# Kernel tuning notes

Hardware: AMD Instinct MI355X
Metric: run time of the kernel (lower is better)

The kernel has to match this reference:

```python
import jax, jax.numpy as jnp
from jax import lax
import numpy as np

MAX_ITER = 200      # hard-coded in DyanEncoder.forward
N_REWEIGHT = 3      # outer reweighting rounds
EPS_W = 0.01


def build_dictionary(rr, theta, T):
    # rows i=0..T-1: [1, rr^i*cos(i*th), (-rr)^i*cos(i*th), rr^i*sin(i*th), (-rr)^i*sin(i*th)]
    i = jnp.arange(T, dtype=rr.dtype)[:, None]          # [T,1]
    pow_p = jnp.power(rr[None, :], i)                   # rr^i, [T,N]
    sign = 1.0 - 2.0 * (jnp.arange(T) % 2).astype(rr.dtype)[:, None]
    pow_m = sign * pow_p                                # (-rr)^i
    c = jnp.cos(i * theta[None, :])
    s = jnp.sin(i * theta[None, :])
    ones = jnp.ones((T, 1), dtype=rr.dtype)
    return jnp.concatenate([ones, pow_p * c, pow_m * c, pow_p * s, pow_m * s], axis=1)  # [T, 1+4N]


def fista_reweighted(D, Y, lam, w):
    # D: [T,K], Y: [B,T,P], w: broadcastable to [B,K,P]
    DtD = D.T @ D                                       # [K,K]
    DtY = jnp.einsum('tk,btp->bkp', D, Y)               # [B,K,P]
    L = jnp.linalg.norm(DtD, ord=2)                     # spectral norm
    Linv = 1.0 / L
    # torch uses Linv.data.item() here -> detached scalar
    w_lam = w * lam * lax.stop_gradient(Linv)
    K = DtD.shape[1]
    A = jnp.eye(K, dtype=D.dtype) - DtD * Linv
    c_minus = DtY * Linv - w_lam
    c_plus = DtY * Linv + w_lam
    x0 = jnp.zeros_like(DtY)

    def step(carry, _):
        x_old, y_old, t_old = carry
        Ay = jnp.einsum('kj,bjp->bkp', A, y_old)
        x_new = jnp.maximum(0.0, Ay + c_minus) + jnp.minimum(0.0, Ay + c_plus)
        t_new = (1.0 + jnp.sqrt(1.0 + 4.0 * t_old ** 2)) / 2.0
        y_new = x_new + ((t_old - 1.0) / t_new) * (x_new - x_old)
        return (x_new, y_new, t_new), None

    (x_fin, _, _), _ = lax.scan(step, (x0, x0, jnp.float32(1.0)), None, length=MAX_ITER)
    return x_fin


def setup_inputs() -> dict:
    key = jax.random.key(0)
    k1, k2, k3 = jax.random.split(key, 3)
    Npoles = 160
    B, T, P = 1, 36, 512
    x = jax.random.normal(k1, (B, T, P), dtype=jnp.float32)
    rr = jax.random.uniform(k2, (Npoles,), dtype=jnp.float32)            # pole magnitudes in (0,1)
    theta = jax.random.uniform(k3, (Npoles,), dtype=jnp.float32) * 3.1415927  # pole angles
    return {"x": x, "rr": rr, "theta": theta, "T": T}


def reference(x, rr, theta, T):
    lam = 0.1
    dic = build_dictionary(rr, theta, T)                # [T, K]
    K = dic.shape[1]
    B, _, P = x.shape
    w = jnp.ones((1, K, P), dtype=x.dtype)
    final = None
    for _ in range(N_REWEIGHT):
        temp = fista_reweighted(dic, x, lam, w)         # [B,K,P]
        wr = 1.0 / (jnp.abs(temp) + EPS_W)
        w = wr / jnp.linalg.norm(wr.reshape(-1))
        final = temp
    return final, dic
```

## Files before the change

kernel.cpp:

```cpp
#include <hip/hip_runtime.h>
#include <math.h>

#define TT 36
#define NP 160
#define KDIM 641
#define PP 512
#define KPAD 704
#define NU 321
#define NSLOT 384
#define BT 512
#define NW 8
#define LAM 0.1f
#define EPSW 0.01f
#define NITER 200
#define NPOW 160

__global__ void k_build_dic(const float* __restrict__ rr, const float* __restrict__ th,
                            float* __restrict__ D, float* __restrict__ outD) {
  int idx = blockIdx.x * blockDim.x + threadIdx.x;
  if (idx >= TT * KDIM) return;
  int t = idx / KDIM, k = idx % KDIM;
  float v;
  if (k == 0) {
    v = 1.0f;
  } else {
    int g = (k - 1) / NP;
    int p = (k - 1) % NP;
    float ft = (float)t;
    float pw = powf(rr[p], ft);
    if ((g == 1 || g == 3) && (t & 1)) pw = -pw;
    float ang = ft * th[p];
    v = pw * ((g < 2) ? cosf(ang) : sinf(ang));
  }
  D[idx] = v;
  outD[idx] = v;
}

__global__ void k_G(const float* __restrict__ D, float* __restrict__ G) {
  int idx = blockIdx.x * blockDim.x + threadIdx.x;
  if (idx >= TT * TT) return;
  int i = idx / TT, j = idx % TT;
  float s = 0.0f;
  for (int k = 0; k < KDIM; ++k) s = fmaf(D[i * KDIM + k], D[j * KDIM + k], s);
  G[idx] = s;
}

__global__ void k_power(const float* __restrict__ G, float* __restrict__ Lb,
                        float* __restrict__ mug) {
  int lane = threadIdx.x;
  float g[TT];
#pragma unroll
  for (int j = 0; j < TT; ++j) g[j] = (lane < TT) ? G[lane * TT + j] : 0.0f;
  float v = (lane < TT) ? 1.0f : 0.0f;
  for (int it = 0; it < NPOW; ++it) {
    float u = 0.0f;
#pragma unroll
    for (int j = 0; j < TT; ++j) u = fmaf(g[j], __shfl(v, j, 64), u);
    float s = u * u;
#pragma unroll
    for (int o = 32; o >= 1; o >>= 1) s += __shfl_xor(s, o, 64);
    v = u * rsqrtf(s);
  }
  float u = 0.0f;
#pragma unroll
  for (int j = 0; j < TT; ++j) u = fmaf(g[j], __shfl(v, j, 64), u);
  float num = v * u, den = v * v;
#pragma unroll
  for (int o = 32; o >= 1; o >>= 1) {
    num += __shfl_xor(num, o, 64);
    den += __shfl_xor(den, o, 64);
  }
  if (lane == 0) {
    float L = num / den;
    Lb[0] = L;
    Lb[1] = 1.0f / L;
    Lb[3] = 0.0f;
    float t = 1.0f;
    for (int i = 0; i < NITER; ++i) {
      float tn = 0.5f * (1.0f + sqrtf(1.0f + 4.0f * t * t));
      mug[i] = (t - 1.0f) / tn;
      t = tn;
    }
  }
}

template <int C>
__device__ __forceinline__ float dppadd(float v) {
  int t = __builtin_amdgcn_update_dpp(0, __float_as_int(v), C, 0xf, 0xf, true);
  return v + __int_as_float(t);
}
__device__ __forceinline__ float wave_sum63(float v) {
  v = dppadd<0xB1>(v);
  v = dppadd<0x4E>(v);
  v = dppadd<0x141>(v);
  v = dppadd<0x140>(v);
  v = dppadd<0x142>(v);
  v = dppadd<0x143>(v);
  return v;
}

__device__ __forceinline__ int colmap(int u) {
  return (u == 0) ? 0 : ((u < 161) ? u : u + 160);
}

__global__ __launch_bounds__(BT, 1) void k_round(
    const float* __restrict__ Dg, const float* __restrict__ X,
    float* __restrict__ Lb, const float* __restrict__ mug,
    const float* __restrict__ xprev, float* __restrict__ xout,
    int first, int last) {
  __shared__ __align__(16) float2 ylds2[NSLOT];
  __shared__ float pbuf[NW * NSLOT];
  __shared__ float muLDS[NITER];
  __shared__ float rn[NW];

  const int tid  = threadIdx.x;
  const int lane = tid & 63;
  const int w    = tid >> 6;
  const float sgn = (w & 1) ? -1.0f : 1.0f;
  const int p    = blockIdx.x;

  const float Linv = Lb[1];
  const float sqL  = sqrtf(Linv);
  const float lamL = LAM * Linv;

  const bool act = (tid < NU);
  const int u    = act ? tid : 0;
  const int kP   = colmap(u);
  const int kM   = (u == 0) ? 0 : kP + 160;

  float Dq[5][6];
#pragma unroll
  for (int i = 0; i < 5; ++i)
#pragma unroll
    for (int j = 0; j < 6; ++j) {
      const int t = w + 8 * i;
      const int ua = lane + 64 * j;
      Dq[i][j] = (t < TT && ua < NU) ? Dg[t * KDIM + colmap(ua)] * sqL : 0.0f;
    }

  float cmP, cpP, cmM, cpM;
  {
    float sE0 = 0.f, sO0 = 0.f;
#pragma unroll 6
    for (int t = 0; t < TT; ++t) {
      const float dv = act ? Dg[t * KDIM + kP] : 0.0f;
      const float xv = X[t * PP + p];
      if (t & 1) sO0 = fmaf(dv, xv, sO0);
      else       sE0 = fmaf(dv, xv, sE0);
    }
    const float c0P = (sE0 + sO0) * Linv, c0M = (sE0 - sO0) * Linv;
    float wlP = lamL, wlM = lamL;
    if (!first) {
      const float nl = lamL * Lb[2];
      wlP = nl / (fabsf(xprev[p * KPAD + kP]) + EPSW);
      wlM = nl / (fabsf(xprev[p * KPAD + ((u > 0) ? kM : kP)]) + EPSW);
    }
    cmP = c0P - wlP; cpP = c0P + wlP;
    cmM = c0M - wlM; cpM = c0M + wlM;
  }

  if (tid < NSLOT) ylds2[tid] = make_float2(0.f, 0.f);
  if (tid < NITER) muLDS[tid] = mug[tid];

  float xP = 0.f, xM = 0.f, yP = 0.f, yM = 0.f;

  __syncthreads();

  for (int it = 0; it < NITER; ++it) {
    float acc[5] = {0.f, 0.f, 0.f, 0.f, 0.f};
#pragma unroll
    for (int j = 0; j < 6; ++j) {
      const float2 yv = ylds2[lane + 64 * j];
      const float op = fmaf(sgn, yv.y, yv.x);
#pragma unroll
      for (int i = 0; i < 5; ++i) acc[i] = fmaf(Dq[i][j], op, acc[i]);
    }
    float z[5];
#pragma unroll
    for (int i = 0; i < 5; ++i) {
      const float r = wave_sum63(acc[i]);
      z[i] = __int_as_float(__builtin_amdgcn_readlane(__float_as_int(r), 63));
    }
#pragma unroll
    for (int j = 0; j < 6; ++j) {
      float pw = Dq[0][j] * z[0];
#pragma unroll
      for (int i = 1; i < 5; ++i) pw = fmaf(Dq[i][j], z[i], pw);
      pbuf[w * NSLOT + lane + 64 * j] = pw;
    }
    __syncthreads();

    const float mu = muLDS[it];
    if (act) {
      const float sE = (pbuf[0 * NSLOT + u] + pbuf[2 * NSLOT + u])
                     + (pbuf[4 * NSLOT + u] + pbuf[6 * NSLOT + u]);
      const float sO = (pbuf[1 * NSLOT + u] + pbuf[3 * NSLOT + u])
                     + (pbuf[5 * NSLOT + u] + pbuf[7 * NSLOT + u]);
      const float sP = sE + sO, sM = sE - sO;
      float uu, xn;
      uu = yP - sP; xn = fmaxf(0.f, uu + cmP) + fminf(0.f, uu + cpP);
      yP = fmaf(mu, xn - xP, xn); xP = xn;
      uu = yM - sM; xn = fmaxf(0.f, uu + cmM) + fminf(0.f, uu + cpM);
      yM = fmaf(mu, xn - xM, xn); xM = xn;
      ylds2[u] = make_float2(yP, (u > 0) ? yM : 0.0f);
    }
    __syncthreads();
  }

  if (act) {
    if (last) {
      xout[kP * PP + p] = xP;
      if (u > 0) xout[kM * PP + p] = xM;
    } else {
      xout[p * KPAD + kP] = xP;
      if (u > 0) xout[p * KPAD + kM] = xM;
    }
  }

  if (!last) {
    float s = 0.0f;
    if (act) {
      const float rP = 1.0f / (fabsf(xP) + EPSW);
      s = rP * rP;
      if (u > 0) { const float rM = 1.0f / (fabsf(xM) + EPSW); s += rM * rM; }
    }
    s = wave_sum63(s);
    if (lane == 63) rn[w] = s;
    __syncthreads();
    if (tid == 0) {
      float tot = 0.f;
#pragma unroll
      for (int i = 0; i < NW; ++i) tot += rn[i];
      atomicAdd(&Lb[3], tot);
    }
  }
}

__global__ void k_norm(float* __restrict__ Lb) {
  if (threadIdx.x == 0) {
    Lb[2] = 1.0f / sqrtf(Lb[3]);
    Lb[3] = 0.0f;
  }
}

extern "C" void kernel_launch(void* const* d_in, const int* in_sizes, int n_in,
                              void* d_out, int out_size, void* d_ws, size_t ws_size,
                              hipStream_t stream) {
  const float* x  = (const float*)d_in[0];
  const float* rr = (const float*)d_in[1];
  const float* th = (const float*)d_in[2];
  float* out = (float*)d_out;
  float* ws  = (float*)d_ws;

  size_t off = 0;
  auto alloc = [&](size_t n) {
    float* p = ws + off;
    off += (n + 63) & ~(size_t)63;
    return p;
  };
  float* D    = alloc((size_t)TT * KDIM);
  float* G    = alloc(TT * TT);
  float* Lb   = alloc(16);
  float* mug  = alloc(NITER);
  float* xa   = alloc((size_t)PP * KPAD);
  if (off * sizeof(float) > ws_size) return;

  k_build_dic<<<(TT * KDIM + 255) / 256, 256, 0, stream>>>(rr, th, D, out + (size_t)KDIM * PP);
  k_G<<<(TT * TT + 255) / 256, 256, 0, stream>>>(D, G);
  k_power<<<1, 64, 0, stream>>>(G, Lb, mug);

  for (int r = 0; r < 3; ++r) {
    const int first = (r == 0), last = (r == 2);
    float* xo = last ? out : xa;
    k_round<<<PP, BT, 0, stream>>>(D, x, Lb, mug, xa, xo, first, last);
    if (!last) k_norm<<<1, 64, 0, stream>>>(Lb);
  }
}
```

Measured before the change: 748.3 us.

## Fuse three reweighting rounds into one persistent kernel with grid barrier

Measured after the change: 825.8 us. 10.3% more time.

```diff
diff --git a/kernel.cpp b/kernel.cpp
--- a/kernel.cpp
+++ b/kernel.cpp
@@ -5,7 +5,6 @@
 #define NP 160
 #define KDIM 641
 #define PP 512
-#define KPAD 704
 #define NU 321
 #define NSLOT 384
 #define BT 512
@@ -75,6 +74,9 @@
     Lb[0] = L;
     Lb[1] = 1.0f / L;
     Lb[3] = 0.0f;
+    Lb[4] = 0.0f;
+    ((unsigned*)(Lb + 8))[0] = 0u;
+    ((unsigned*)(Lb + 8))[1] = 0u;
     float t = 1.0f;
     for (int i = 0; i < NITER; ++i) {
       float tn = 0.5f * (1.0f + sqrtf(1.0f + 4.0f * t * t));
@@ -103,15 +105,15 @@
   return (u == 0) ? 0 : ((u < 161) ? u : u + 160);
 }
 
-__global__ __launch_bounds__(BT, 1) void k_round(
+__global__ __launch_bounds__(BT, 4) void k_fused(
     const float* __restrict__ Dg, const float* __restrict__ X,
     float* __restrict__ Lb, const float* __restrict__ mug,
-    const float* __restrict__ xprev, float* __restrict__ xout,
-    int first, int last) {
+    float* __restrict__ out) {
   __shared__ __align__(16) float2 ylds2[NSLOT];
   __shared__ float pbuf[NW * NSLOT];
   __shared__ float muLDS[NITER];
   __shared__ float rn[NW];
+  __shared__ float nrmsh;
 
   const int tid  = threadIdx.x;
   const int lane = tid & 63;
@@ -138,7 +140,7 @@
       Dq[i][j] = (t < TT && ua < NU) ? Dg[t * KDIM + colmap(ua)] * sqL : 0.0f;
     }
 
-  float cmP, cpP, cmM, cpM;
+  float c0P, c0M;
   {
     float sE0 = 0.f, sO0 = 0.f;
 #pragma unroll 6
@@ -148,98 +150,103 @@
       if (t & 1) sO0 = fmaf(dv, xv, sO0);
       else       sE0 = fmaf(dv, xv, sE0);
     }
-    const float c0P = (sE0 + sO0) * Linv, c0M = (sE0 - sO0) * Linv;
-    float wlP = lamL, wlM = lamL;
-    if (!first) {
-      const float nl = lamL * Lb[2];
-      wlP = nl / (fabsf(xprev[p * KPAD + kP]) + EPSW);
-      wlM = nl / (fabsf(xprev[p * KPAD + ((u > 0) ? kM : kP)]) + EPSW);
-    }
-    cmP = c0P - wlP; cpP = c0P + wlP;
-    cmM = c0M - wlM; cpM = c0M + wlM;
-  }
-
-  if (tid < NSLOT) ylds2[tid] = make_float2(0.f, 0.f);
+    c0P = (sE0 + sO0) * Linv;
+    c0M = (sE0 - sO0) * Linv;
+  }
+
   if (tid < NITER) muLDS[tid] = mug[tid];
 
   float xP = 0.f, xM = 0.f, yP = 0.f, yM = 0.f;
-
-  __syncthreads();
-
-  for (int it = 0; it < NITER; ++it) {
-    float acc[5] = {0.f, 0.f, 0.f, 0.f, 0.f};
-#pragma unroll
-    for (int j = 0; j < 6; ++j) {
-      const float2 yv = ylds2[lane + 64 * j];
-      const float op = fmaf(sgn, yv.y, yv.x);
-#pragma unroll
-      for (int i = 0; i < 5; ++i) acc[i] = fmaf(Dq[i][j], op, acc[i]);
-    }
-    float z[5];
-#pragma unroll
-    for (int i = 0; i < 5; ++i) {
-      const float r = wave_sum63(acc[i]);
-      z[i] = __int_as_float(__builtin_amdgcn_readlane(__float_as_int(r), 63));
-    }
-#pragma unroll
-    for (int j = 0; j < 6; ++j) {
-      float pw = Dq[0][j] * z[0];
-#pragma unroll
-      for (int i = 1; i < 5; ++i) pw = fmaf(Dq[i][j], z[i], pw);
-      pbuf[w * NSLOT + lane + 64 * j] = pw;
-    }
+  float rninv = 0.f;
+
+  for (int r = 0; r < 3; ++r) {
+    float wlP, wlM;
+    if (r == 0) {
+      wlP = lamL; wlM = lamL;
+    } else {
+      const float nl = lamL * rninv;
+      wlP = nl / (fabsf(xP) + EPSW);
+      wlM = nl / (fabsf((u > 0) ? xM : xP) + EPSW);
+    }
+    const float cmP = c0P - wlP, cpP = c0P + wlP;
+    const float cmM = c0M - wlM, cpM = c0M + wlM;
+    xP = 0.f; xM = 0.f; yP = 0.f; yM = 0.f;
+    if (tid < NSLOT) ylds2[tid] = make_float2(0.f, 0.f);
     __syncthreads();
 
-    const float mu = muLDS[it];
-    if (act) {
-      const float sE = (pbuf[0 * NSLOT + u] + pbuf[2 * NSLOT + u])
-                     + (pbuf[4 * NSLOT + u] + pbuf[6 * NSLOT + u]);
-      const float sO = (pbuf[1 * NSLOT + u] + pbuf[3 * NSLOT + u])
-                     + (pbuf[5 * NSLOT + u] + pbuf[7 * NSLOT + u]);
-      const float sP = sE + sO, sM = sE - sO;
-      float uu, xn;
-      uu = yP - sP; xn = fmaxf(0.f, uu + cmP) + fminf(0.f, uu + cpP);
-      yP = fmaf(mu, xn - xP, xn); xP = xn;
-      uu = yM - sM; xn = fmaxf(0.f, uu + cmM) + fminf(0.f, uu + cpM);
-      yM = fmaf(mu, xn - xM, xn); xM = xn;
-      ylds2[u] = make_float2(yP, (u > 0) ? yM : 0.0f);
-    }
-    __syncthreads();
+    for (int it = 0; it < NITER; ++it) {
+      float acc[5] = {0.f, 0.f, 0.f, 0.f, 0.f};
+#pragma unroll
+      for (int j = 0; j < 6; ++j) {
+        const float2 yv = ylds2[lane + 64 * j];
+        const float op = fmaf(sgn, yv.y, yv.x);
+#pragma unroll
+        for (int i = 0; i < 5; ++i) acc[i] = fmaf(Dq[i][j], op, acc[i]);
+      }
+      float z[5];
+#pragma unroll
+      for (int i = 0; i < 5; ++i) {
+        const float rr_ = wave_sum63(acc[i]);
+        z[i] = __int_as_float(__builtin_amdgcn_readlane(__float_as_int(rr_), 63));
+      }
+#pragma unroll
+      for (int j = 0; j < 6; ++j) {
+        float pw = Dq[0][j] * z[0];
+#pragma unroll
+        for (int i = 1; i < 5; ++i) pw = fmaf(Dq[i][j], z[i], pw);
+        pbuf[w * NSLOT + lane + 64 * j] = pw;
+      }
+      __syncthreads();
+
+      const float mu = muLDS[it];
+      if (act) {
+        const float sE = (pbuf[0 * NSLOT + u] + pbuf[2 * NSLOT + u])
+                       + (pbuf[4 * NSLOT + u] + pbuf[6 * NSLOT + u]);
+        const float sO = (pbuf[1 * NSLOT + u] + pbuf[3 * NSLOT + u])
+                       + (pbuf[5 * NSLOT + u] + pbuf[7 * NSLOT + u]);
+        const float sP = sE + sO, sM = sE - sO;
+        float uu, xn;
+        uu = yP - sP; xn = fmaxf(0.f, uu + cmP) + fminf(0.f, uu + cpP);
+        yP = fmaf(mu, xn - xP, xn); xP = xn;
+        uu = yM - sM; xn = fmaxf(0.f, uu + cmM) + fminf(0.f, uu + cpM);
+        yM = fmaf(mu, xn - xM, xn); xM = xn;
+        ylds2[u] = make_float2(yP, (u > 0) ? yM : 0.0f);
+      }
+      __syncthreads();
+    }
+
+    if (r < 2) {
+      float s = 0.0f;
+      if (act) {
+        const float rP = 1.0f / (fabsf(xP) + EPSW);
+        s = rP * rP;
+        if (u > 0) { const float rM = 1.0f / (fabsf(xM) + EPSW); s += rM * rM; }
+      }
+      s = wave_sum63(s);
+      if (lane == 63) rn[w] = s;
+      __syncthreads();
+      if (tid == 0) {
+        float tot = 0.f;
+#pragma unroll
+        for (int i = 0; i < NW; ++i) tot += rn[i];
+        __hip_atomic_fetch_add(&Lb[3 + r], tot, __ATOMIC_RELEASE, __HIP_MEMORY_SCOPE_AGENT);
+        unsigned* cnt = (unsigned*)(Lb + 8) + r;
+        __hip_atomic_fetch_add(cnt, 1u, __ATOMIC_ACQ_REL, __HIP_MEMORY_SCOPE_AGENT);
+        unsigned spins = 0;
+        while (__hip_atomic_load(cnt, __ATOMIC_ACQUIRE, __HIP_MEMORY_SCOPE_AGENT) < (unsigned)PP) {
+          if (++spins > 100000000u) break;
+          __builtin_amdgcn_s_sleep(8);
+        }
+        nrmsh = __hip_atomic_load(&Lb[3 + r], __ATOMIC_RELAXED, __HIP_MEMORY_SCOPE_AGENT);
+      }
+      __syncthreads();
+      rninv = rsqrtf(nrmsh);
+    }
   }
 
   if (act) {
-    if (last) {
-      xout[kP * PP + p] = xP;
-      if (u > 0) xout[kM * PP + p] = xM;
-    } else {
-      xout[p * KPAD + kP] = xP;
-      if (u > 0) xout[p * KPAD + kM] = xM;
-    }
-  }
-
-  if (!last) {
-    float s = 0.0f;
-    if (act) {
-      const float rP = 1.0f / (fabsf(xP) + EPSW);
-      s = rP * rP;
-      if (u > 0) { const float rM = 1.0f / (fabsf(xM) + EPSW); s += rM * rM; }
-    }
-    s = wave_sum63(s);
-    if (lane == 63) rn[w] = s;
-    __syncthreads();
-    if (tid == 0) {
-      float tot = 0.f;
-#pragma unroll
-      for (int i = 0; i < NW; ++i) tot += rn[i];
-      atomicAdd(&Lb[3], tot);
-    }
-  }
-}
-
-__global__ void k_norm(float* __restrict__ Lb) {
-  if (threadIdx.x == 0) {
-    Lb[2] = 1.0f / sqrtf(Lb[3]);
-    Lb[3] = 0.0f;
+    out[kP * PP + p] = xP;
+    if (u > 0) out[kM * PP + p] = xM;
   }
 }
 
@@ -262,17 +269,10 @@
   float* G    = alloc(TT * TT);
   float* Lb   = alloc(16);
   float* mug  = alloc(NITER);
-  float* xa   = alloc((size_t)PP * KPAD);
   if (off * sizeof(float) > ws_size) return;
 
   k_build_dic<<<(TT * KDIM + 255) / 256, 256, 0, stream>>>(rr, th, D, out + (size_t)KDIM * PP);
   k_G<<<(TT * TT + 255) / 256, 256, 0, stream>>>(D, G);
   k_power<<<1, 64, 0, stream>>>(G, Lb, mug);
-
-  for (int r = 0; r < 3; ++r) {
-    const int first = (r == 0), last = (r == 2);
-    float* xo = last ? out : xa;
-    k_round<<<PP, BT, 0, stream>>>(D, x, Lb, mug, xa, xo, first, last);
-    if (!last) k_norm<<<1, 64, 0, stream>>>(Lb);
-  }
-}
+  k_fused<<<PP, BT, 0, stream>>>(D, x, Lb, mug, out);
+}
```
